# Optimization experiments

Hardware: AMD Instinct MI355X
Metric: run time of the kernel (lower is better)

The kernel has to match this reference:

```python
import jax, jax.numpy as jnp
import numpy as np

N, E = 100000, 1600000
IN_D, HID, OUT_D = 64, 64, 16
BN_EPS = 1e-5


def setup_inputs() -> dict:
    key = jax.random.key(0)
    ks = list(jax.random.split(key, 32))
    k = iter(ks)
    inp = {}
    inp["x"] = jax.random.normal(next(k), (N, IN_D), dtype=jnp.float32)
    inp["edge_index"] = jax.random.randint(next(k), (2, E), 0, N, dtype=jnp.int64)
    def lin(kk, fan_in, fan_out):
        s = 1.0 / np.sqrt(fan_in)
        return jax.random.uniform(kk, (fan_in, fan_out), jnp.float32, -s, s)
    for i, ind in ((1, IN_D), (2, HID), (3, HID)):
        inp[f"eps{i}"] = jnp.zeros((), jnp.float32)
        inp[f"w{i}1"] = lin(next(k), ind, HID)
        inp[f"b{i}1"] = jnp.zeros((HID,), jnp.float32)
        inp[f"w{i}2"] = lin(next(k), HID, HID)
        inp[f"b{i}2"] = jnp.zeros((HID,), jnp.float32)
        inp[f"g{i}"] = jnp.ones((HID,), jnp.float32)
        inp[f"bt{i}"] = jnp.zeros((HID,), jnp.float32)
    inp["wl"] = lin(next(k), HID, OUT_D)
    inp["bl"] = jnp.zeros((OUT_D,), jnp.float32)
    return inp


def _gin_conv(x, src, dst, eps, w1, b1, w2, b2, g, bt):
    # scatter-add neighbor sum: agg[i] = sum_{(s->i) in E} x[s]
    agg = jax.ops.segment_sum(x[src], dst, num_segments=N)
    h = (1.0 + eps) * x + agg
    h = jax.nn.relu(h @ w1 + b1)
    h = jax.nn.relu(h @ w2 + b2)
    # BatchNorm1d over nodes (training mode: batch stats, biased variance)
    mu = jnp.mean(h, axis=0)
    var = jnp.var(h, axis=0)
    h = (h - mu) * jax.lax.rsqrt(var + BN_EPS) * g + bt
    return h


def reference(x, edge_index,
              eps1, w11, b11, w12, b12, g1, bt1,
              eps2, w21, b21, w22, b22, g2, bt2,
              eps3, w31, b31, w32, b32, g3, bt3,
              wl, bl):
    src, dst = edge_index[0], edge_index[1]
    h = jax.nn.relu(_gin_conv(x, src, dst, eps1, w11, b11, w12, b12, g1, bt1))
    h = jax.nn.relu(_gin_conv(h, src, dst, eps2, w21, b21, w22, b22, g2, bt2))
    h = jax.nn.relu(_gin_conv(h, src, dst, eps3, w31, b31, w32, b32, g3, bt3))
    return h @ wl + bl
```

## Files before the change

### kernel.cpp

```cpp
#include <hip/hip_runtime.h>
#include <hip/hip_fp16.h>
#include <math.h>

#define N_NODES 100000
#define NB 1563
#define BN_EPS 1e-5f
#define PART_BLOCKS 128

__global__ void zero_misc_k(float* stats, int* gcnt) {
    int gid = blockIdx.x * blockDim.x + threadIdx.x;
    if (gid < 384) stats[gid] = 0.f;
    if (gid < NB) gcnt[gid] = 0;
}

__global__ void tofp16_k(const float* __restrict__ x, __half* __restrict__ xh, int n4) {
    int gid = blockIdx.x * blockDim.x + threadIdx.x;
    if (gid >= n4) return;
    float4 v = reinterpret_cast<const float4*>(x)[gid];
    union { float2 f; __half2 h[2]; } u;
    u.h[0] = __float22half2_rn(make_float2(v.x, v.y));
    u.h[1] = __float22half2_rn(make_float2(v.z, v.w));
    reinterpret_cast<float2*>(xh)[gid] = u.f;
}

__global__ __launch_bounds__(256) void histA_k(const int* __restrict__ ei,
                                               int* __restrict__ gcnt, int E) {
    __shared__ int cnt[NB];
    for (int i = threadIdx.x; i < NB; i += 256) cnt[i] = 0;
    __syncthreads();
    int per = (E + gridDim.x - 1) / gridDim.x;
    int s0 = blockIdx.x * per, s1 = min(E, s0 + per);
    for (int e = s0 + threadIdx.x; e < s1; e += 256)
        atomicAdd(&cnt[ei[E + e] >> 6], 1);
    __syncthreads();
    for (int i = threadIdx.x; i < NB; i += 256)
        if (cnt[i]) atomicAdd(&gcnt[i], cnt[i]);
}

__global__ __launch_bounds__(256) void scanA_k(const int* __restrict__ gcnt,
                                               int* __restrict__ bbase,
                                               int* __restrict__ gcursor) {
    __shared__ int tmp[256];
    int t = threadIdx.x;
    int v[7];
    int s = 0;
#pragma unroll
    for (int j = 0; j < 7; ++j) {
        int idx = t * 7 + j;
        v[j] = (idx < NB) ? gcnt[idx] : 0;
        s += v[j];
    }
    tmp[t] = s;
    __syncthreads();
    for (int off = 1; off < 256; off <<= 1) {
        int a = (t >= off) ? tmp[t - off] : 0;
        __syncthreads();
        tmp[t] += a;
        __syncthreads();
    }
    int run = tmp[t] - s;
#pragma unroll
    for (int j = 0; j < 7; ++j) {
        int idx = t * 7 + j;
        if (idx < NB) { bbase[idx] = run; gcursor[idx] = run; }
        run += v[j];
    }
    if (t == 255) bbase[NB] = run;
}

__global__ __launch_bounds__(256) void partA_k(const int* __restrict__ ei,
                                               int* __restrict__ gcursor,
                                               int* __restrict__ part, int E) {
    __shared__ int cnt[NB];
    __shared__ int base[NB];
    for (int i = threadIdx.x; i < NB; i += 256) cnt[i] = 0;
    __syncthreads();
    int per = (E + gridDim.x - 1) / gridDim.x;
    int s0 = blockIdx.x * per, s1 = min(E, s0 + per);
    for (int e = s0 + threadIdx.x; e < s1; e += 256)
        atomicAdd(&cnt[ei[E + e] >> 6], 1);
    __syncthreads();
    for (int i = threadIdx.x; i < NB; i += 256) {
        int c = cnt[i];
        base[i] = c ? atomicAdd(&gcursor[i], c) : 0;
    }
    __syncthreads();
    for (int i = threadIdx.x; i < NB; i += 256) cnt[i] = 0;
    __syncthreads();
    for (int e = s0 + threadIdx.x; e < s1; e += 256) {
        int s = ei[e], d = ei[E + e];
        int b = d >> 6, dl = d & 63;
        int lo = atomicAdd(&cnt[b], 1);
        part[base[b] + lo] = (dl << 20) | s;
    }
}

__global__ __launch_bounds__(256) void sortB_k(const int* __restrict__ part,
                                               const int* __restrict__ bbase,
                                               int* __restrict__ row_ptr,
                                               int* __restrict__ csr_src) {
    __shared__ int cnt[64];
    __shared__ int cur[64];
    int b = blockIdx.x;
    int t = threadIdx.x;
    int e0 = bbase[b], e1 = bbase[b + 1];
    if (t < 64) cnt[t] = 0;
    __syncthreads();
    for (int i = e0 + t; i < e1; i += 256) atomicAdd(&cnt[(part[i] >> 20) & 63], 1);
    __syncthreads();
    if (t < 64) {
        int c = cnt[t];
        int v = c;
        for (int off = 1; off < 64; off <<= 1) {
            int u = __shfl_up(v, off, 64);
            if (t >= off) v += u;
        }
        int excl = v - c;
        int node = b * 64 + t;
        if (node <= N_NODES) row_ptr[node] = e0 + excl;
        cur[t] = e0 + excl;
    }
    __syncthreads();
    for (int i = e0 + t; i < e1; i += 256) {
        int u = part[i];
        int dl = (u >> 20) & 63;
        int pos = atomicAdd(&cur[dl], 1);
        csr_src[pos] = u & 0xFFFFF;
    }
}

__device__ __forceinline__ float4 ld_row16(const __half* __restrict__ base, int cg) {
    float2 raw = reinterpret_cast<const float2*>(base)[cg];
    __half2 h01 = *reinterpret_cast<const __half2*>(&raw.x);
    __half2 h23 = *reinterpret_cast<const __half2*>(&raw.y);
    float2 f01 = __half22float2(h01);
    float2 f23 = __half22float2(h23);
    return make_float4(f01.x, f01.y, f23.x, f23.y);
}

template <bool FIRST>
__global__ __launch_bounds__(256, 6) void layer_k(
    const __half* __restrict__ hin, const float* __restrict__ pstats,
    const float* __restrict__ pg, const float* __restrict__ pbt,
    const int* __restrict__ row_ptr, const int* __restrict__ csr_src,
    const float* __restrict__ epsp,
    const float* __restrict__ w1, const float* __restrict__ b1,
    const float* __restrict__ w2, const float* __restrict__ b2,
    __half* __restrict__ hout, float* __restrict__ stats) {
    __shared__ float xs[64][68];
    __shared__ float ssc[64], sof[64];
    __shared__ float sred[128];

    int tid = threadIdx.x;
    int r0 = blockIdx.x * 64;

    if (tid < 64) {
        if (FIRST) {
            ssc[tid] = 1.f;
            sof[tid] = 0.f;
        } else {
            float mean = pstats[tid] * (1.f / N_NODES);
            float var = pstats[64 + tid] * (1.f / N_NODES) - mean * mean;
            float sc = pg[tid] * rsqrtf(var + BN_EPS);
            ssc[tid] = sc;
            sof[tid] = pbt[tid] - mean * sc;
        }
    }
    if (tid < 128) sred[tid] = 0.f;
    __syncthreads();

    float eps1 = 1.0f + *epsp;
    int cg = tid & 15;
    float s0 = ssc[cg * 4 + 0], s1 = ssc[cg * 4 + 1];
    float s2 = ssc[cg * 4 + 2], s3 = ssc[cg * 4 + 3];
    float o0 = sof[cg * 4 + 0], o1 = sof[cg * 4 + 1];
    float o2 = sof[cg * 4 + 2], o3 = sof[cg * 4 + 3];

#define BNRELU(u)                                   \
    if (!FIRST) {                                   \
        u.x = fmaxf(fmaf(u.x, s0, o0), 0.f);        \
        u.y = fmaxf(fmaf(u.y, s1, o1), 0.f);        \
        u.z = fmaxf(fmaf(u.z, s2, o2), 0.f);        \
        u.w = fmaxf(fmaf(u.w, s3, o3), 0.f);        \
    }

    {
        int rr = tid >> 4;
#pragma unroll
        for (int i = 0; i < 4; ++i) {
            int r = rr + i * 16;
            int node = r0 + r;
            float4 acc = make_float4(0.f, 0.f, 0.f, 0.f);
            if (node < N_NODES) {
                float4 v = ld_row16(hin + (size_t)node * 64, cg);
                BNRELU(v);
                acc.x = v.x * eps1; acc.y = v.y * eps1;
                acc.z = v.z * eps1; acc.w = v.w * eps1;
                int j0 = row_ptr[node], j1 = row_ptr[node + 1];
                int j = j0;
                for (; j + 4 <= j1; j += 4) {
                    int ia = csr_src[j + 0];
                    int ib = csr_src[j + 1];
                    int ic = csr_src[j + 2];
                    int id = csr_src[j + 3];
                    float4 ua = ld_row16(hin + (size_t)ia * 64, cg);
                    float4 ub = ld_row16(hin + (size_t)ib * 64, cg);
                    float4 uc = ld_row16(hin + (size_t)ic * 64, cg);
                    float4 ud = ld_row16(hin + (size_t)id * 64, cg);
                    BNRELU(ua); BNRELU(ub); BNRELU(uc); BNRELU(ud);
                    acc.x += ua.x + ub.x + uc.x + ud.x;
                    acc.y += ua.y + ub.y + uc.y + ud.y;
                    acc.z += ua.z + ub.z + uc.z + ud.z;
                    acc.w += ua.w + ub.w + uc.w + ud.w;
                }
                for (; j < j1; ++j) {
                    int sidx = csr_src[j];
                    float4 u = ld_row16(hin + (size_t)sidx * 64, cg);
                    BNRELU(u);
                    acc.x += u.x; acc.y += u.y; acc.z += u.z; acc.w += u.w;
                }
            }
            xs[cg * 4 + 0][r] = acc.x;
            xs[cg * 4 + 1][r] = acc.y;
            xs[cg * 4 + 2][r] = acc.z;
            xs[cg * 4 + 3][r] = acc.w;
        }
    }
#undef BNRELU
    __syncthreads();

    int tr = tid & 15, tc = tid >> 4;
    int r = tr * 4, c = tc * 4;
    float acc[4][4];
    const float4* w14 = reinterpret_cast<const float4*>(w1);
    const float4* w24 = reinterpret_cast<const float4*>(w2);

#pragma unroll
    for (int i = 0; i < 4; ++i)
#pragma unroll
        for (int j = 0; j < 4; ++j) acc[i][j] = 0.f;
#pragma unroll 4
    for (int k = 0; k < 64; ++k) {
        float4 xv = *reinterpret_cast<const float4*>(&xs[k][r]);
        float4 wv = w14[k * 16 + tc];
        float xa[4] = {xv.x, xv.y, xv.z, xv.w};
        float wa[4] = {wv.x, wv.y, wv.z, wv.w};
#pragma unroll
        for (int i = 0; i < 4; ++i)
#pragma unroll
            for (int j = 0; j < 4; ++j) acc[i][j] = fmaf(xa[i], wa[j], acc[i][j]);
    }
    {
        float4 bv = reinterpret_cast<const float4*>(b1)[tc];
        float ba[4] = {bv.x, bv.y, bv.z, bv.w};
#pragma unroll
        for (int j = 0; j < 4; ++j)
#pragma unroll
            for (int i = 0; i < 4; ++i) acc[i][j] = fmaxf(acc[i][j] + ba[j], 0.f);
    }
    __syncthreads();

#pragma unroll
    for (int i = 0; i < 4; ++i)
#pragma unroll
        for (int j = 0; j < 4; ++j) xs[c + j][r + i] = acc[i][j];
    __syncthreads();

#pragma unroll
    for (int i = 0; i < 4; ++i)
#pragma unroll
        for (int j = 0; j < 4; ++j) acc[i][j] = 0.f;
#pragma unroll 4
    for (int k = 0; k < 64; ++k) {
        float4 xv = *reinterpret_cast<const float4*>(&xs[k][r]);
        float4 wv = w24[k * 16 + tc];
        float xa[4] = {xv.x, xv.y, xv.z, xv.w};
        float wa[4] = {wv.x, wv.y, wv.z, wv.w};
#pragma unroll
        for (int i = 0; i < 4; ++i)
#pragma unroll
            for (int j = 0; j < 4; ++j) acc[i][j] = fmaf(xa[i], wa[j], acc[i][j]);
    }
    {
        float4 bv = reinterpret_cast<const float4*>(b2)[tc];
        float ba[4] = {bv.x, bv.y, bv.z, bv.w};
#pragma unroll
        for (int j = 0; j < 4; ++j)
#pragma unroll
            for (int i = 0; i < 4; ++i) acc[i][j] = fmaxf(acc[i][j] + ba[j], 0.f);
    }

#pragma unroll
    for (int i = 0; i < 4; ++i) {
        int row = r0 + r + i;
        if (row < N_NODES) {
            union { float2 f; __half2 h[2]; } u;
            u.h[0] = __float22half2_rn(make_float2(acc[i][0], acc[i][1]));
            u.h[1] = __float22half2_rn(make_float2(acc[i][2], acc[i][3]));
            *reinterpret_cast<float2*>(hout + (size_t)row * 64 + c) = u.f;
        }
    }
#pragma unroll
    for (int j = 0; j < 4; ++j) {
        float s = 0.f, q = 0.f;
#pragma unroll
        for (int i = 0; i < 4; ++i) {
            if (r0 + r + i < N_NODES) {
                s += acc[i][j];
                q += acc[i][j] * acc[i][j];
            }
        }
        atomicAdd(&sred[c + j], s);
        atomicAdd(&sred[64 + c + j], q);
    }
    __syncthreads();
    if (tid < 128) atomicAdd(&stats[tid], sred[tid]);
}

__global__ __launch_bounds__(256) void final_k(const __half* __restrict__ hin,
                                               const float* __restrict__ pstats,
                                               const float* __restrict__ pg,
                                               const float* __restrict__ pbt,
                                               const float* __restrict__ wl,
                                               const float* __restrict__ bl,
                                               float* __restrict__ out) {
    __shared__ float xs[64][68];
    __shared__ float wsh[64 * 16];
    __shared__ float bsh[16];
    __shared__ float ssc[64], sof[64];
    int tid = threadIdx.x;
    int r0 = blockIdx.x * 64;

    if (tid < 64) {
        float mean = pstats[tid] * (1.f / N_NODES);
        float var = pstats[64 + tid] * (1.f / N_NODES) - mean * mean;
        float sc = pg[tid] * rsqrtf(var + BN_EPS);
        ssc[tid] = sc;
        sof[tid] = pbt[tid] - mean * sc;
    }
    reinterpret_cast<float4*>(wsh)[tid] = reinterpret_cast<const float4*>(wl)[tid];
    if (tid < 16) bsh[tid] = bl[tid];
    __syncthreads();

    {
        int rr = tid >> 4, cg = tid & 15;
#pragma unroll
        for (int i = 0; i < 4; ++i) {
            int r = rr + i * 16;
            float4 v = make_float4(0.f, 0.f, 0.f, 0.f);
            if (r0 + r < N_NODES) {
                v = ld_row16(hin + (size_t)(r0 + r) * 64, cg);
                int c = cg * 4;
                v.x = fmaxf(fmaf(v.x, ssc[c + 0], sof[c + 0]), 0.f);
                v.y = fmaxf(fmaf(v.y, ssc[c + 1], sof[c + 1]), 0.f);
                v.z = fmaxf(fmaf(v.z, ssc[c + 2], sof[c + 2]), 0.f);
                v.w = fmaxf(fmaf(v.w, ssc[c + 3], sof[c + 3]), 0.f);
            }
            xs[cg * 4 + 0][r] = v.x;
            xs[cg * 4 + 1][r] = v.y;
            xs[cg * 4 + 2][r] = v.z;
            xs[cg * 4 + 3][r] = v.w;
        }
    }
    __syncthreads();

    int tc = tid & 3, r = tid >> 2;
    int c = tc * 4;
    float acc0 = 0.f, acc1 = 0.f, acc2 = 0.f, acc3 = 0.f;
#pragma unroll 8
    for (int k = 0; k < 64; ++k) {
        float xv = xs[k][r];
        float4 wv = *reinterpret_cast<const float4*>(&wsh[k * 16 + c]);
        acc0 = fmaf(xv, wv.x, acc0);
        acc1 = fmaf(xv, wv.y, acc1);
        acc2 = fmaf(xv, wv.z, acc2);
        acc3 = fmaf(xv, wv.w, acc3);
    }
    int row = r0 + r;
    if (row < N_NODES) {
        float4 o = make_float4(acc0 + bsh[c], acc1 + bsh[c + 1], acc2 + bsh[c + 2], acc3 + bsh[c + 3]);
        *reinterpret_cast<float4*>(out + (size_t)row * 16 + c) = o;
    }
}

extern "C" void kernel_launch(void* const* d_in, const int* in_sizes, int n_in,
                              void* d_out, int out_size, void* d_ws, size_t ws_size,
                              hipStream_t stream) {
    const float* x = (const float*)d_in[0];
    const int* ei = (const int*)d_in[1];
    const int E = in_sizes[1] / 2;

    const float* eps[3] = {(const float*)d_in[2], (const float*)d_in[9], (const float*)d_in[16]};
    const float* w1[3]  = {(const float*)d_in[3], (const float*)d_in[10], (const float*)d_in[17]};
    const float* b1[3]  = {(const float*)d_in[4], (const float*)d_in[11], (const float*)d_in[18]};
    const float* w2[3]  = {(const float*)d_in[5], (const float*)d_in[12], (const float*)d_in[19]};
    const float* b2[3]  = {(const float*)d_in[6], (const float*)d_in[13], (const float*)d_in[20]};
    const float* g[3]   = {(const float*)d_in[7], (const float*)d_in[14], (const float*)d_in[21]};
    const float* bt[3]  = {(const float*)d_in[8], (const float*)d_in[15], (const float*)d_in[22]};
    const float* wl = (const float*)d_in[23];
    const float* bl = (const float*)d_in[24];

    __half* xh   = (__half*)d_ws;
    __half* ha   = xh + (size_t)N_NODES * 64;
    __half* hb   = ha + (size_t)N_NODES * 64;
    float* stats = (float*)(hb + (size_t)N_NODES * 64);
    int* gcnt    = (int*)(stats + 384);
    int* bbase   = gcnt + NB;
    int* gcursor = bbase + (NB + 1);
    int* row_ptr = gcursor + NB;
    int* tail    = row_ptr + (N_NODES + 1);
    size_t used  = (size_t)((char*)tail - (char*)d_ws);

    int* csr_src;
    int* part;
    if (used + 2 * (size_t)E * 4 <= ws_size) {
        csr_src = tail;
        part = csr_src + E;
    } else {
        part = tail;
        csr_src = (int*)d_out;
    }

    const int n4 = N_NODES * 16;

    zero_misc_k<<<(NB + 255) / 256, 256, 0, stream>>>(stats, gcnt);
    tofp16_k<<<(n4 + 255) / 256, 256, 0, stream>>>(x, xh, n4);
    histA_k<<<PART_BLOCKS, 256, 0, stream>>>(ei, gcnt, E);
    scanA_k<<<1, 256, 0, stream>>>(gcnt, bbase, gcursor);
    partA_k<<<PART_BLOCKS, 256, 0, stream>>>(ei, gcursor, part, E);
    sortB_k<<<NB, 256, 0, stream>>>(part, bbase, row_ptr, csr_src);

    layer_k<true><<<NB, 256, 0, stream>>>(xh, nullptr, nullptr, nullptr, row_ptr, csr_src,
                                          eps[0], w1[0], b1[0], w2[0], b2[0], ha, stats + 0);
    layer_k<false><<<NB, 256, 0, stream>>>(ha, stats + 0, g[0], bt[0], row_ptr, csr_src,
                                           eps[1], w1[1], b1[1], w2[1], b2[1], hb, stats + 128);
    layer_k<false><<<NB, 256, 0, stream>>>(hb, stats + 128, g[1], bt[1], row_ptr, csr_src,
                                           eps[2], w1[2], b1[2], w2[2], b2[2], ha, stats + 256);

    final_k<<<NB, 256, 0, stream>>>(ha, stats + 256, g[2], bt[2], wl, bl, (float*)d_out);
}
```

Measured before the change: 373.2 us.

## Apply BN+ReLU once per node in separate pass, use half2 gather sums

Moves the batchnorm and ReLU of each layer's output out of the neighbor gather loop into a standalone elementwise kernel. Each node's row is then normalized once instead of once per incoming edge. The gather now adds four neighbor rows in half precision before converting to float. The node tile per block is halved to 32 rows with 128-thread blocks, which removes bounds checks because 100000 divides evenly by 32. The cost is three extra elementwise passes over the hidden activations and some loss of accumulation precision from the fp16 adds.

```diff
diff --git a/kernel.cpp b/kernel.cpp
--- a/kernel.cpp
+++ b/kernel.cpp
@@ -3,7 +3,8 @@
 #include <math.h>
 
 #define N_NODES 100000
-#define NB 1563
+#define ROWS 32
+#define NB 3125
 #define BN_EPS 1e-5f
 #define PART_BLOCKS 128
 
@@ -31,7 +32,7 @@
     int per = (E + gridDim.x - 1) / gridDim.x;
     int s0 = blockIdx.x * per, s1 = min(E, s0 + per);
     for (int e = s0 + threadIdx.x; e < s1; e += 256)
-        atomicAdd(&cnt[ei[E + e] >> 6], 1);
+        atomicAdd(&cnt[ei[E + e] >> 5], 1);
     __syncthreads();
     for (int i = threadIdx.x; i < NB; i += 256)
         if (cnt[i]) atomicAdd(&gcnt[i], cnt[i]);
@@ -42,11 +43,11 @@
                                                int* __restrict__ gcursor) {
     __shared__ int tmp[256];
     int t = threadIdx.x;
-    int v[7];
+    int v[13];
     int s = 0;
 #pragma unroll
-    for (int j = 0; j < 7; ++j) {
-        int idx = t * 7 + j;
+    for (int j = 0; j < 13; ++j) {
+        int idx = t * 13 + j;
         v[j] = (idx < NB) ? gcnt[idx] : 0;
         s += v[j];
     }
@@ -60,8 +61,8 @@
     }
     int run = tmp[t] - s;
 #pragma unroll
-    for (int j = 0; j < 7; ++j) {
-        int idx = t * 7 + j;
+    for (int j = 0; j < 13; ++j) {
+        int idx = t * 13 + j;
         if (idx < NB) { bbase[idx] = run; gcursor[idx] = run; }
         run += v[j];
     }
@@ -78,7 +79,7 @@
     int per = (E + gridDim.x - 1) / gridDim.x;
     int s0 = blockIdx.x * per, s1 = min(E, s0 + per);
     for (int e = s0 + threadIdx.x; e < s1; e += 256)
-        atomicAdd(&cnt[ei[E + e] >> 6], 1);
+        atomicAdd(&cnt[ei[E + e] >> 5], 1);
     __syncthreads();
     for (int i = threadIdx.x; i < NB; i += 256) {
         int c = cnt[i];
@@ -89,7 +90,7 @@
     __syncthreads();
     for (int e = s0 + threadIdx.x; e < s1; e += 256) {
         int s = ei[e], d = ei[E + e];
-        int b = d >> 6, dl = d & 63;
+        int b = d >> 5, dl = d & 31;
         int lo = atomicAdd(&cnt[b], 1);
         part[base[b] + lo] = (dl << 20) | s;
     }
@@ -99,137 +100,103 @@
                                                const int* __restrict__ bbase,
                                                int* __restrict__ row_ptr,
                                                int* __restrict__ csr_src) {
-    __shared__ int cnt[64];
-    __shared__ int cur[64];
+    __shared__ int cnt[ROWS];
+    __shared__ int cur[ROWS];
     int b = blockIdx.x;
     int t = threadIdx.x;
     int e0 = bbase[b], e1 = bbase[b + 1];
-    if (t < 64) cnt[t] = 0;
-    __syncthreads();
-    for (int i = e0 + t; i < e1; i += 256) atomicAdd(&cnt[(part[i] >> 20) & 63], 1);
-    __syncthreads();
-    if (t < 64) {
+    if (t < ROWS) cnt[t] = 0;
+    __syncthreads();
+    for (int i = e0 + t; i < e1; i += 256) atomicAdd(&cnt[(part[i] >> 20) & 31], 1);
+    __syncthreads();
+    if (t < ROWS) {
         int c = cnt[t];
         int v = c;
-        for (int off = 1; off < 64; off <<= 1) {
-            int u = __shfl_up(v, off, 64);
+        for (int off = 1; off < ROWS; off <<= 1) {
+            int u = __shfl_up(v, off, ROWS);
             if (t >= off) v += u;
         }
         int excl = v - c;
-        int node = b * 64 + t;
-        if (node <= N_NODES) row_ptr[node] = e0 + excl;
+        row_ptr[b * ROWS + t] = e0 + excl;
         cur[t] = e0 + excl;
     }
+    if (t == ROWS && b == NB - 1) row_ptr[N_NODES] = e1;
     __syncthreads();
     for (int i = e0 + t; i < e1; i += 256) {
         int u = part[i];
-        int dl = (u >> 20) & 63;
+        int dl = (u >> 20) & 31;
         int pos = atomicAdd(&cur[dl], 1);
         csr_src[pos] = u & 0xFFFFF;
     }
 }
 
-__device__ __forceinline__ float4 ld_row16(const __half* __restrict__ base, int cg) {
-    float2 raw = reinterpret_cast<const float2*>(base)[cg];
-    __half2 h01 = *reinterpret_cast<const __half2*>(&raw.x);
-    __half2 h23 = *reinterpret_cast<const __half2*>(&raw.y);
-    float2 f01 = __half22float2(h01);
-    float2 f23 = __half22float2(h23);
-    return make_float4(f01.x, f01.y, f23.x, f23.y);
-}
-
-template <bool FIRST>
-__global__ __launch_bounds__(256, 6) void layer_k(
-    const __half* __restrict__ hin, const float* __restrict__ pstats,
-    const float* __restrict__ pg, const float* __restrict__ pbt,
+__global__ __launch_bounds__(128, 8) void layer_k(
+    const __half* __restrict__ hin,
     const int* __restrict__ row_ptr, const int* __restrict__ csr_src,
     const float* __restrict__ epsp,
     const float* __restrict__ w1, const float* __restrict__ b1,
     const float* __restrict__ w2, const float* __restrict__ b2,
     __half* __restrict__ hout, float* __restrict__ stats) {
-    __shared__ float xs[64][68];
-    __shared__ float ssc[64], sof[64];
+    __shared__ float xs[64][36];
     __shared__ float sred[128];
 
     int tid = threadIdx.x;
-    int r0 = blockIdx.x * 64;
-
-    if (tid < 64) {
-        if (FIRST) {
-            ssc[tid] = 1.f;
-            sof[tid] = 0.f;
-        } else {
-            float mean = pstats[tid] * (1.f / N_NODES);
-            float var = pstats[64 + tid] * (1.f / N_NODES) - mean * mean;
-            float sc = pg[tid] * rsqrtf(var + BN_EPS);
-            ssc[tid] = sc;
-            sof[tid] = pbt[tid] - mean * sc;
-        }
-    }
+    int r0 = blockIdx.x * ROWS;
     if (tid < 128) sred[tid] = 0.f;
-    __syncthreads();
 
     float eps1 = 1.0f + *epsp;
     int cg = tid & 15;
-    float s0 = ssc[cg * 4 + 0], s1 = ssc[cg * 4 + 1];
-    float s2 = ssc[cg * 4 + 2], s3 = ssc[cg * 4 + 3];
-    float o0 = sof[cg * 4 + 0], o1 = sof[cg * 4 + 1];
-    float o2 = sof[cg * 4 + 2], o3 = sof[cg * 4 + 3];
-
-#define BNRELU(u)                                   \
-    if (!FIRST) {                                   \
-        u.x = fmaxf(fmaf(u.x, s0, o0), 0.f);        \
-        u.y = fmaxf(fmaf(u.y, s1, o1), 0.f);        \
-        u.z = fmaxf(fmaf(u.z, s2, o2), 0.f);        \
-        u.w = fmaxf(fmaf(u.w, s3, o3), 0.f);        \
-    }
-
-    {
-        int rr = tid >> 4;
-#pragma unroll
-        for (int i = 0; i < 4; ++i) {
-            int r = rr + i * 16;
-            int node = r0 + r;
-            float4 acc = make_float4(0.f, 0.f, 0.f, 0.f);
-            if (node < N_NODES) {
-                float4 v = ld_row16(hin + (size_t)node * 64, cg);
-                BNRELU(v);
-                acc.x = v.x * eps1; acc.y = v.y * eps1;
-                acc.z = v.z * eps1; acc.w = v.w * eps1;
-                int j0 = row_ptr[node], j1 = row_ptr[node + 1];
-                int j = j0;
-                for (; j + 4 <= j1; j += 4) {
-                    int ia = csr_src[j + 0];
-                    int ib = csr_src[j + 1];
-                    int ic = csr_src[j + 2];
-                    int id = csr_src[j + 3];
-                    float4 ua = ld_row16(hin + (size_t)ia * 64, cg);
-                    float4 ub = ld_row16(hin + (size_t)ib * 64, cg);
-                    float4 uc = ld_row16(hin + (size_t)ic * 64, cg);
-                    float4 ud = ld_row16(hin + (size_t)id * 64, cg);
-                    BNRELU(ua); BNRELU(ub); BNRELU(uc); BNRELU(ud);
-                    acc.x += ua.x + ub.x + uc.x + ud.x;
-                    acc.y += ua.y + ub.y + uc.y + ud.y;
-                    acc.z += ua.z + ub.z + uc.z + ud.z;
-                    acc.w += ua.w + ub.w + uc.w + ud.w;
-                }
-                for (; j < j1; ++j) {
-                    int sidx = csr_src[j];
-                    float4 u = ld_row16(hin + (size_t)sidx * 64, cg);
-                    BNRELU(u);
-                    acc.x += u.x; acc.y += u.y; acc.z += u.z; acc.w += u.w;
-                }
-            }
-            xs[cg * 4 + 0][r] = acc.x;
-            xs[cg * 4 + 1][r] = acc.y;
-            xs[cg * 4 + 2][r] = acc.z;
-            xs[cg * 4 + 3][r] = acc.w;
+    int rr = tid >> 4;
+
+    union F2H { float2 f; __half2 h[2]; };
+
+#pragma unroll
+    for (int i = 0; i < 4; ++i) {
+        int r = rr + i * 8;
+        int node = r0 + r;
+        const float2* selfp = reinterpret_cast<const float2*>(hin + (size_t)node * 64);
+        F2H sv; sv.f = selfp[cg];
+        float2 f0 = __half22float2(sv.h[0]);
+        float2 f1 = __half22float2(sv.h[1]);
+        float4 acc = make_float4(f0.x * eps1, f0.y * eps1, f1.x * eps1, f1.y * eps1);
+
+        int j0 = row_ptr[node], j1 = row_ptr[node + 1];
+        int j = j0;
+        for (; j + 4 <= j1; j += 4) {
+            int ia = csr_src[j + 0];
+            int ib = csr_src[j + 1];
+            int ic = csr_src[j + 2];
+            int id = csr_src[j + 3];
+            F2H a, b, c, d;
+            a.f = reinterpret_cast<const float2*>(hin + (size_t)ia * 64)[cg];
+            b.f = reinterpret_cast<const float2*>(hin + (size_t)ib * 64)[cg];
+            c.f = reinterpret_cast<const float2*>(hin + (size_t)ic * 64)[cg];
+            d.f = reinterpret_cast<const float2*>(hin + (size_t)id * 64)[cg];
+            __half2 p0 = __hadd2(a.h[0], b.h[0]);
+            __half2 p1 = __hadd2(a.h[1], b.h[1]);
+            __half2 q0 = __hadd2(c.h[0], d.h[0]);
+            __half2 q1 = __hadd2(c.h[1], d.h[1]);
+            __half2 s0 = __hadd2(p0, q0);
+            __half2 s1 = __hadd2(p1, q1);
+            float2 g0 = __half22float2(s0);
+            float2 g1 = __half22float2(s1);
+            acc.x += g0.x; acc.y += g0.y; acc.z += g1.x; acc.w += g1.y;
         }
-    }
-#undef BNRELU
-    __syncthreads();
-
-    int tr = tid & 15, tc = tid >> 4;
+        for (; j < j1; ++j) {
+            int sidx = csr_src[j];
+            F2H u; u.f = reinterpret_cast<const float2*>(hin + (size_t)sidx * 64)[cg];
+            float2 g0 = __half22float2(u.h[0]);
+            float2 g1 = __half22float2(u.h[1]);
+            acc.x += g0.x; acc.y += g0.y; acc.z += g1.x; acc.w += g1.y;
+        }
+        xs[cg * 4 + 0][r] = acc.x;
+        xs[cg * 4 + 1][r] = acc.y;
+        xs[cg * 4 + 2][r] = acc.z;
+        xs[cg * 4 + 3][r] = acc.w;
+    }
+    __syncthreads();
+
+    int tr = tid & 7, tc = tid >> 3;
     int r = tr * 4, c = tc * 4;
     float acc[4][4];
     const float4* w14 = reinterpret_cast<const float4*>(w1);
@@ -293,22 +260,18 @@
 #pragma unroll
     for (int i = 0; i < 4; ++i) {
         int row = r0 + r + i;
-        if (row < N_NODES) {
-            union { float2 f; __half2 h[2]; } u;
-            u.h[0] = __float22half2_rn(make_float2(acc[i][0], acc[i][1]));
-            u.h[1] = __float22half2_rn(make_float2(acc[i][2], acc[i][3]));
-            *reinterpret_cast<float2*>(hout + (size_t)row * 64 + c) = u.f;
-        }
+        union { float2 f; __half2 h[2]; } u;
+        u.h[0] = __float22half2_rn(make_float2(acc[i][0], acc[i][1]));
+        u.h[1] = __float22half2_rn(make_float2(acc[i][2], acc[i][3]));
+        *reinterpret_cast<float2*>(hout + (size_t)row * 64 + c) = u.f;
     }
 #pragma unroll
     for (int j = 0; j < 4; ++j) {
         float s = 0.f, q = 0.f;
 #pragma unroll
         for (int i = 0; i < 4; ++i) {
-            if (r0 + r + i < N_NODES) {
-                s += acc[i][j];
-                q += acc[i][j] * acc[i][j];
-            }
+            s += acc[i][j];
+            q += acc[i][j] * acc[i][j];
         }
         atomicAdd(&sred[c + j], s);
         atomicAdd(&sred[64 + c + j], q);
@@ -317,30 +280,48 @@
     if (tid < 128) atomicAdd(&stats[tid], sred[tid]);
 }
 
+__global__ __launch_bounds__(256) void bnrelu_k(const __half* hin,
+                                                const float* __restrict__ stats,
+                                                const float* __restrict__ g,
+                                                const float* __restrict__ bt,
+                                                __half* hout) {
+    __shared__ float ssc[64], sof[64];
+    int tid = threadIdx.x;
+    if (tid < 64) {
+        float mean = stats[tid] * (1.f / N_NODES);
+        float var = stats[64 + tid] * (1.f / N_NODES) - mean * mean;
+        float sc = g[tid] * rsqrtf(var + BN_EPS);
+        ssc[tid] = sc;
+        sof[tid] = bt[tid] - mean * sc;
+    }
+    __syncthreads();
+    int gid = blockIdx.x * 256 + tid;
+    if (gid >= N_NODES * 8) return;
+    int c0 = (gid & 7) * 8;
+    union { float4 f; __half2 h[4]; } u;
+    u.f = reinterpret_cast<const float4*>(hin)[gid];
+#pragma unroll
+    for (int q = 0; q < 4; ++q) {
+        float2 v = __half22float2(u.h[q]);
+        v.x = fmaxf(fmaf(v.x, ssc[c0 + 2 * q], sof[c0 + 2 * q]), 0.f);
+        v.y = fmaxf(fmaf(v.y, ssc[c0 + 2 * q + 1], sof[c0 + 2 * q + 1]), 0.f);
+        u.h[q] = __float22half2_rn(v);
+    }
+    reinterpret_cast<float4*>(hout)[gid] = u.f;
+}
+
 __global__ __launch_bounds__(256) void final_k(const __half* __restrict__ hin,
-                                               const float* __restrict__ pstats,
-                                               const float* __restrict__ pg,
-                                               const float* __restrict__ pbt,
                                                const float* __restrict__ wl,
                                                const float* __restrict__ bl,
                                                float* __restrict__ out) {
     __shared__ float xs[64][68];
     __shared__ float wsh[64 * 16];
     __shared__ float bsh[16];
-    __shared__ float ssc[64], sof[64];
     int tid = threadIdx.x;
     int r0 = blockIdx.x * 64;
 
-    if (tid < 64) {
-        float mean = pstats[tid] * (1.f / N_NODES);
-        float var = pstats[64 + tid] * (1.f / N_NODES) - mean * mean;
-        float sc = pg[tid] * rsqrtf(var + BN_EPS);
-        ssc[tid] = sc;
-        sof[tid] = pbt[tid] - mean * sc;
-    }
     reinterpret_cast<float4*>(wsh)[tid] = reinterpret_cast<const float4*>(wl)[tid];
     if (tid < 16) bsh[tid] = bl[tid];
-    __syncthreads();
 
     {
         int rr = tid >> 4, cg = tid & 15;
@@ -349,12 +330,11 @@
             int r = rr + i * 16;
             float4 v = make_float4(0.f, 0.f, 0.f, 0.f);
             if (r0 + r < N_NODES) {
-                v = ld_row16(hin + (size_t)(r0 + r) * 64, cg);
-                int c = cg * 4;
-                v.x = fmaxf(fmaf(v.x, ssc[c + 0], sof[c + 0]), 0.f);
-                v.y = fmaxf(fmaf(v.y, ssc[c + 1], sof[c + 1]), 0.f);
-                v.z = fmaxf(fmaf(v.z, ssc[c + 2], sof[c + 2]), 0.f);
-                v.w = fmaxf(fmaf(v.w, ssc[c + 3], sof[c + 3]), 0.f);
+                union { float2 f; __half2 h[2]; } u;
+                u.f = reinterpret_cast<const float2*>(hin + (size_t)(r0 + r) * 64)[cg];
+                float2 f0 = __half22float2(u.h[0]);
+                float2 f1 = __half22float2(u.h[1]);
+                v = make_float4(f0.x, f0.y, f1.x, f1.y);
             }
             xs[cg * 4 + 0][r] = v.x;
             xs[cg * 4 + 1][r] = v.y;
@@ -430,12 +410,19 @@
     partA_k<<<PART_BLOCKS, 256, 0, stream>>>(ei, gcursor, part, E);
     sortB_k<<<NB, 256, 0, stream>>>(part, bbase, row_ptr, csr_src);
 
-    layer_k<true><<<NB, 256, 0, stream>>>(xh, nullptr, nullptr, nullptr, row_ptr, csr_src,
-                                          eps[0], w1[0], b1[0], w2[0], b2[0], ha, stats + 0);
-    layer_k<false><<<NB, 256, 0, stream>>>(ha, stats + 0, g[0], bt[0], row_ptr, csr_src,
-                                           eps[1], w1[1], b1[1], w2[1], b2[1], hb, stats + 128);
-    layer_k<false><<<NB, 256, 0, stream>>>(hb, stats + 128, g[1], bt[1], row_ptr, csr_src,
-                                           eps[2], w1[2], b1[2], w2[2], b2[2], ha, stats + 256);
-
-    final_k<<<NB, 256, 0, stream>>>(ha, stats + 256, g[2], bt[2], wl, bl, (float*)d_out);
-}
+    const int bnblk = (N_NODES * 8 + 255) / 256;
+
+    layer_k<<<NB, 128, 0, stream>>>(xh, row_ptr, csr_src, eps[0],
+                                    w1[0], b1[0], w2[0], b2[0], ha, stats + 0);
+    bnrelu_k<<<bnblk, 256, 0, stream>>>(ha, stats + 0, g[0], bt[0], ha);
+
+    layer_k<<<NB, 128, 0, stream>>>(ha, row_ptr, csr_src, eps[1],
+                                    w1[1], b1[1], w2[1], b2[1], hb, stats + 128);
+    bnrelu_k<<<bnblk, 256, 0, stream>>>(hb, stats + 128, g[1], bt[1], hb);
+
+    layer_k<<<NB, 128, 0, stream>>>(hb, row_ptr, csr_src, eps[2],
+                                    w1[2], b1[2], w2[2], b2[2], ha, stats + 256);
+    bnrelu_k<<<bnblk, 256, 0, stream>>>(ha, stats + 256, g[2], bt[2], ha);
+
+    final_k<<<(N_NODES + 63) / 64, 256, 0, stream>>>(ha, wl, bl, (float*)d_out);
+}
```

New measurement: 483.1 us. 1.29x slower.
